# Performance work log

Measured on AMD Instinct MI355X. Metric: run time of the kernel, lower is better.

## Reference

```python
import jax, jax.numpy as jnp
import numpy as np

EPS = 1e-12  # F.normalize eps


def setup_inputs() -> dict:
    key = jax.random.key(0)
    ks = jax.random.split(key, 12)
    N_NODES, N_EDGES, VOCAB, D = 100000, 1600000, 200000, 128
    return {
        "ent_embs": jax.random.normal(ks[0], (VOCAB, D), dtype=jnp.float32),
        "rel_embs": jax.random.normal(ks[1], (500, D), dtype=jnp.float32),
        "e_r_bias": jax.random.normal(ks[2], (N_NODES, D), dtype=jnp.float32),
        "out_norm": jax.random.uniform(ks[3], (N_NODES, 1), dtype=jnp.float32),
        "weight_neighbor": jax.random.normal(ks[4], (D, D), dtype=jnp.float32) * 0.05,
        "gru_w_ih": jax.random.normal(ks[5], (3 * D, 2 * D), dtype=jnp.float32) * 0.05,
        "gru_w_hh": jax.random.normal(ks[6], (3 * D, D), dtype=jnp.float32) * 0.05,
        "gru_b_ih": jnp.zeros((3 * D,), dtype=jnp.float32),
        "gru_b_hh": jnp.zeros((3 * D,), dtype=jnp.float32),
        "node_id": jax.random.randint(ks[7], (N_NODES,), 0, VOCAB, dtype=jnp.int64) if jax.config.jax_enable_x64 else jax.random.randint(ks[7], (N_NODES,), 0, VOCAB).astype(jnp.int32),
        "edge_src": jax.random.randint(ks[8], (N_EDGES,), 0, N_NODES).astype(jnp.int32),
        "edge_dst": jax.random.randint(ks[9], (N_EDGES,), 0, N_NODES).astype(jnp.int32),
        "g_idx": 0,
    }


def gru_cell(x, h, w_ih, w_hh, b_ih, b_hh):
    # torch.nn.GRUCell semantics; gates stacked as [r, z, n]
    gx = x @ w_ih.T + b_ih            # [N, 3D]
    gh = h @ w_hh.T + b_hh            # [N, 3D]
    xr, xz, xn = jnp.split(gx, 3, axis=1)
    hr, hz, hn = jnp.split(gh, 3, axis=1)
    r = jax.nn.sigmoid(xr + hr)
    z = jax.nn.sigmoid(xz + hz)
    n = jnp.tanh(xn + r * hn)
    return (1.0 - z) * n + z * h


def reference(ent_embs, rel_embs, e_r_bias, out_norm, weight_neighbor,
              gru_w_ih, gru_w_hh, gru_b_ih, gru_b_hh,
              node_id, edge_src, edge_dst, g_idx):
    n_nodes = e_r_bias.shape[0]
    # gather node embeddings, transform once per node (equivalent to per-edge mm)
    h = ent_embs[node_id]                       # [N, D]
    hW = h @ weight_neighbor                    # [N, D]
    msg = hW[edge_src]                          # [E, D] per-edge message
    agg = jax.ops.segment_sum(msg, edge_dst, num_segments=n_nodes)  # scatter-sum
    agg = agg * out_norm                        # apply_func: elementwise norm scale
    x = jnp.concatenate([agg, e_r_bias], axis=1)  # [N, 2D]
    # g_idx == 0 branch: hidden state is e_r_bias
    h0 = gru_cell(x, e_r_bias, gru_w_ih, gru_w_hh, gru_b_ih, gru_b_hh)
    h0 = jax.nn.relu(h0)
    # dropout is identity in eval mode
    norm = jnp.maximum(jnp.linalg.norm(h0, axis=1, keepdims=True), EPS)
    return h0 / norm
```

## Files before the change

### kernel.cpp

```cpp
#include <hip/hip_runtime.h>
#include <hip/hip_bf16.h>

#define D 128

typedef unsigned short u16;
typedef unsigned int   u32;
typedef unsigned long long u64;
typedef short bf16x8 __attribute__((ext_vector_type(8)));
typedef float f32x4  __attribute__((ext_vector_type(4)));

__device__ __forceinline__ float bf2f(u16 u) {
    union { u32 i; float f; } v; v.i = ((u32)u) << 16; return v.f;
}
__device__ __forceinline__ float bflo(u32 p) {
    union { u32 i; float f; } v; v.i = p << 16; return v.f;
}
__device__ __forceinline__ float bfhi(u32 p) {
    union { u32 i; float f; } v; v.i = p & 0xffff0000u; return v.f;
}
__device__ __forceinline__ u16 f2bf(float f) {
    union { float f; u32 i; } v; v.f = f;
    return (u16)((v.i + 0x7fffu + ((v.i >> 16) & 1u)) >> 16);
}
__device__ __forceinline__ float ldf(const void* p, long i, int isb) {
    return isb ? bf2f(((const u16*)p)[i]) : ((const float*)p)[i];
}

__device__ __forceinline__ float sigm(float x) { return 1.0f / (1.0f + __expf(-x)); }
__device__ __forceinline__ float tanh_fast(float x) {
    float a = fabsf(x);
    float t = __expf(-2.0f * a);
    float r = (1.0f - t) / (1.0f + t);
    return copysignf(r, x);
}

__global__ void DRlocal_net_79173427135059_kernel() {}

__global__ __launch_bounds__(64) void k_detect(const void* ent, const void* nid,
                                               int* flag, int* bhist) {
    int lane = threadIdx.x;
    for (int i = lane; i < 512; i += 64) bhist[i] = 0;
    float a = fabsf(bf2f(((const u16*)ent)[lane]));
    bool sane = (a >= 9.765625e-4f && a <= 64.0f);
    u64 m = __ballot(sane);
    u32 w = ((const u32*)nid)[lane];
    bool oddzero = ((lane & 1) == 0) || (w == 0u);
    u64 m2 = __ballot(oddzero);
    if (lane == 0) {
        flag[0] = (__popcll(m) >= 48) ? 1 : 0;
        flag[1] = (m2 == ~0ull) ? 1 : 0;
    }
}

__global__ __launch_bounds__(256) void k_prep(
    const void* __restrict__ w_ih, const void* __restrict__ w_hh,
    const void* __restrict__ b_ih, const void* __restrict__ b_hh,
    const void* __restrict__ W, const int* __restrict__ flag,
    u16* __restrict__ WTb, u16* __restrict__ Wihb, u16* __restrict__ Whhb,
    float* __restrict__ bif, float* __restrict__ bhf)
{
    int isb = flag[0];
    int t = blockIdx.x * 256 + threadIdx.x;
    if (t < 16384) {
        int k = t >> 7, j = t & 127;
        u16 v = isb ? ((const u16*)W)[t] : f2bf(((const float*)W)[t]);
        WTb[j * 128 + k] = v;
        return;
    }
    int u = t - 16384;
    if (u < 98304) { Wihb[u] = isb ? ((const u16*)w_ih)[u] : f2bf(((const float*)w_ih)[u]); return; }
    int v = u - 98304;
    if (v < 49152) { Whhb[v] = isb ? ((const u16*)w_hh)[v] : f2bf(((const float*)w_hh)[v]); return; }
    int b = v - 49152;
    if (b < 384) { bif[b] = ldf(b_ih, b, isb); return; }
    int c = b - 384;
    if (c < 384) { bhf[c] = ldf(b_hh, c, isb); return; }
}

__global__ __launch_bounds__(256) void k_gmm_mfma(
    const void* __restrict__ ent, const void* __restrict__ node_id,
    const u16* __restrict__ WTb, u16* __restrict__ hW,
    const int* __restrict__ flag, int N)
{
    int isb = flag[0], i64 = flag[1];
    int tid = threadIdx.x;
    int wave = tid >> 6, lane = tid & 63;
    int qm = lane >> 4, qr = lane & 15;
    int row0 = blockIdx.x * 64 + wave * 16;

    int rowA = row0 + qr; if (rowA >= N) rowA = N - 1;
    long nid = i64 ? (long)((const long long*)node_id)[rowA]
                   : (long)((const int*)node_id)[rowA];

    bf16x8 a[4];
    if (isb) {
        const u16* ep = (const u16*)ent + nid * 128 + qm * 8;
        #pragma unroll
        for (int s = 0; s < 4; ++s) a[s] = *(const bf16x8*)(ep + s * 32);
    } else {
        const float* ep = (const float*)ent + nid * 128 + qm * 8;
        #pragma unroll
        for (int s = 0; s < 4; ++s) {
            float4 f0 = *(const float4*)(ep + s * 32);
            float4 f1 = *(const float4*)(ep + s * 32 + 4);
            bf16x8 t;
            t[0] = (short)f2bf(f0.x); t[1] = (short)f2bf(f0.y);
            t[2] = (short)f2bf(f0.z); t[3] = (short)f2bf(f0.w);
            t[4] = (short)f2bf(f1.x); t[5] = (short)f2bf(f1.y);
            t[6] = (short)f2bf(f1.z); t[7] = (short)f2bf(f1.w);
            a[s] = t;
        }
    }

    int r0 = row0 + qm * 4;
    #pragma unroll
    for (int f = 0; f < 8; ++f) {
        f32x4 acc = {0.f, 0.f, 0.f, 0.f};
        const u16* wp = WTb + (size_t)(f * 16 + qr) * 128 + qm * 8;
        #pragma unroll
        for (int s = 0; s < 4; ++s) {
            bf16x8 b = *(const bf16x8*)(wp + s * 32);
            acc = __builtin_amdgcn_mfma_f32_16x16x32_bf16(a[s], b, acc, 0, 0, 0);
        }
        int col = f * 16 + qr;
        #pragma unroll
        for (int r = 0; r < 4; ++r) {
            int row = r0 + r;
            if (row < N) hW[(size_t)row * 128 + col] = f2bf(acc[r]);
        }
    }
}


__global__ __launch_bounds__(256) void k_bhist(
    const int* __restrict__ edst, int* __restrict__ bhist,
    int E, int NB, int bshift)
{
    __shared__ int lcnt[512];
    int t = threadIdx.x;
    int e0 = blockIdx.x * 8192;
    for (int i = t; i < NB; i += 256) lcnt[i] = 0;
    __syncthreads();
    for (int i = t; i < 8192; i += 256) {
        int e = e0 + i;
        if (e < E) atomicAdd(&lcnt[edst[e] >> bshift], 1);
    }
    __syncthreads();
    for (int i = t; i < NB; i += 256) {
        int c = lcnt[i];
        if (c) atomicAdd(&bhist[i], c);
    }
}

__global__ __launch_bounds__(512) void k_bscan(
    const int* __restrict__ bhist, int* __restrict__ bstart,
    int* __restrict__ bcur, int* __restrict__ rowstart,
    int NB, int N, int E)
{
    __shared__ int sh[512];
    int t = threadIdx.x;
    int v = (t < NB) ? bhist[t] : 0;
    sh[t] = v;
    __syncthreads();
    #pragma unroll
    for (int off = 1; off < 512; off <<= 1) {
        int x = (t >= off) ? sh[t - off] : 0;
        __syncthreads();
        sh[t] += x;
        __syncthreads();
    }
    int excl = sh[t] - v;
    if (t < NB) { bstart[t] = excl; bcur[t] = excl; }
    if (t == 0) { bstart[NB] = E; rowstart[N] = E; }
}

__global__ __launch_bounds__(256) void k_afill(
    const int* __restrict__ esrc, const int* __restrict__ edst,
    int* __restrict__ bcur, u64* __restrict__ ebuf,
    int E, int NB, int bshift)
{
    __shared__ int lcnt[512];
    int t = threadIdx.x;
    int e0 = blockIdx.x * 8192;
    for (int i = t; i < NB; i += 256) lcnt[i] = 0;
    __syncthreads();
    for (int i = t; i < 8192; i += 256) {
        int e = e0 + i;
        if (e < E) atomicAdd(&lcnt[edst[e] >> bshift], 1);
    }
    __syncthreads();
    for (int b = t; b < NB; b += 256) {
        int c = lcnt[b];
        lcnt[b] = c ? atomicAdd(&bcur[b], c) : 0;
    }
    __syncthreads();
    for (int i = t; i < 8192; i += 256) {
        int e = e0 + i;
        if (e < E) {
            int d = edst[e];
            int pos = atomicAdd(&lcnt[d >> bshift], 1);
            ebuf[pos] = ((u64)(u32)esrc[e] << 32) | (u32)d;
        }
    }
}

__global__ __launch_bounds__(256) void k_bfill(
    const u64* __restrict__ ebuf, const int* __restrict__ bstart,
    int* __restrict__ rowstart, int* __restrict__ sorted_src,
    int N, int bshift)
{
    __shared__ int lcnt[1024];
    __shared__ int lscan[256];
    int b = blockIdx.x, t = threadIdx.x;
    int nodes = 1 << bshift;
    int per = nodes >> 8;
    int base = b << bshift;
    int beg = bstart[b], end = bstart[b + 1];

    for (int i = t; i < nodes; i += 256) lcnt[i] = 0;
    __syncthreads();
    for (int i = beg + t; i < end; i += 256) {
        int d = (int)(u32)ebuf[i];
        atomicAdd(&lcnt[d - base], 1);
    }
    __syncthreads();

    int myv[4]; int mysum = 0;
    #pragma unroll
    for (int j = 0; j < 4; ++j) {
        myv[j] = (j < per) ? lcnt[t * per + j] : 0;
        mysum += myv[j];
    }
    lscan[t] = mysum;
    __syncthreads();
    #pragma unroll
    for (int off = 1; off < 256; off <<= 1) {
        int x = (t >= off) ? lscan[t - off] : 0;
        __syncthreads();
        lscan[t] += x;
        __syncthreads();
    }
    int run = beg + lscan[t] - mysum;
    #pragma unroll
    for (int j = 0; j < 4; ++j) {
        if (j < per) {
            int idx = t * per + j;
            int node = base + idx;
            if (node < N) rowstart[node] = run;
            lcnt[idx] = run;
            run += myv[j];
        }
    }
    __syncthreads();
    for (int i = beg + t; i < end; i += 256) {
        u64 p = ebuf[i];
        int d = (int)(u32)p;
        int pos = atomicAdd(&lcnt[d - base], 1);
        sorted_src[pos] = (int)(p >> 32);
    }
}

__global__ __launch_bounds__(256) void k_seg(
    const u16* __restrict__ hW, const int* __restrict__ rowstart,
    const int* __restrict__ sorted_src, const void* __restrict__ onorm,
    const void* __restrict__ bias, u16* __restrict__ X,
    const int* __restrict__ flag, int N)
{
    int isb = flag[0];
    int tid = threadIdx.x;
    int node = blockIdx.x * 4 + (tid >> 6);
    int lane = tid & 63;
    if (node >= N) return;
    int beg = rowstart[node], end = rowstart[node + 1];
    const u32* hw2 = (const u32*)hW;
    float a0 = 0.f, a1 = 0.f;
    int e = beg;
    for (; e + 8 <= end; e += 8) {
        int sI[8]; u32 vI[8];
        #pragma unroll
        for (int i = 0; i < 8; ++i) sI[i] = sorted_src[e + i];
        #pragma unroll
        for (int i = 0; i < 8; ++i) vI[i] = hw2[(size_t)sI[i] * 64 + lane];
        #pragma unroll
        for (int i = 0; i < 8; ++i) { a0 += bflo(vI[i]); a1 += bfhi(vI[i]); }
    }
    for (; e + 4 <= end; e += 4) {
        int s0 = sorted_src[e], s1 = sorted_src[e + 1];
        int s2 = sorted_src[e + 2], s3 = sorted_src[e + 3];
        u32 v0 = hw2[(size_t)s0 * 64 + lane];
        u32 v1 = hw2[(size_t)s1 * 64 + lane];
        u32 v2 = hw2[(size_t)s2 * 64 + lane];
        u32 v3 = hw2[(size_t)s3 * 64 + lane];
        a0 += bflo(v0) + bflo(v1) + bflo(v2) + bflo(v3);
        a1 += bfhi(v0) + bfhi(v1) + bfhi(v2) + bfhi(v3);
    }
    for (; e < end; ++e) {
        u32 v = hw2[(size_t)sorted_src[e] * 64 + lane];
        a0 += bflo(v); a1 += bfhi(v);
    }
    float on = ldf(onorm, node, isb);
    u32 p = ((u32)f2bf(a1 * on) << 16) | (u32)f2bf(a0 * on);
    ((u32*)X)[(size_t)node * 128 + lane] = p;
    u32 pb;
    if (isb) pb = ((const u32*)bias)[(size_t)node * 64 + lane];
    else {
        const float* bp = (const float*)bias + (size_t)node * 128 + lane * 2;
        pb = ((u32)f2bf(bp[1]) << 16) | (u32)f2bf(bp[0]);
    }
    ((u32*)X)[(size_t)node * 128 + 64 + lane] = pb;
}

__global__ __launch_bounds__(512, 2) void k_gru_mfma(
    const u16* __restrict__ X, const u16* __restrict__ Wih,
    const u16* __restrict__ Whh, const float* __restrict__ bif,
    const float* __restrict__ bhf, void* __restrict__ out,
    float* __restrict__ ssb,
    const int* __restrict__ flag, int N, int NpadX)
{
    __shared__ alignas(16) char smem[147456];
    int isb = flag[0];
    int tid = threadIdx.x;
    int wave = tid >> 6, lane = tid & 63;
    int qm = lane >> 4, qr = lane & 15;
    int g = blockIdx.x & 1;
    int chunk = blockIdx.x >> 1;
    int g64 = g * 64;

    for (int t = tid; t < 6144; t += 512) {
        int L = t * 16;
        int kb = L & 511;
        int c  = (L >> 9) & 63;
        int gi = L >> 15;
        int src = (gi * 128 + g64 + c) * 512 + kb;
        int dst = L ^ ((c & 7) << 4);
        *(bf16x8*)(smem + dst) = *(const bf16x8*)((const char*)Wih + src);
    }
    for (int t = tid; t < 3072; t += 512) {
        int L = t * 16;
        int kb = L & 255;
        int c  = (L >> 8) & 63;
        int gi = L >> 14;
        int src = (gi * 128 + g64 + c) * 256 + kb;
        int dst = 98304 + (L ^ ((c & 7) << 4));
        *(bf16x8*)(smem + dst) = *(const bf16x8*)((const char*)Whh + src);
    }
    __syncthreads();

    int rbase = chunk * 256 + wave * 32;

    bf16x8 aA[8], aB[8];
    {
        const u16* x0 = X + (size_t)(rbase + qr) * 256 + qm * 8;
        #pragma unroll
        for (int s = 0; s < 8; ++s) aA[s] = *(const bf16x8*)(x0 + s * 32);
        const u16* x1 = x0 + 16 * 256;
        #pragma unroll
        for (int s = 0; s < 8; ++s) aB[s] = *(const bf16x8*)(x1 + s * 32);
    }

    float ss[8] = {0.f, 0.f, 0.f, 0.f, 0.f, 0.f, 0.f, 0.f};

    #pragma unroll 1
    for (int sl = 0; sl < 4; ++sl) {
        int colIdx = sl * 16 + qr;
        int colg = g64 + colIdx;
        int sw = (qr & 7) << 4;
        int cbI = colIdx * 512 + qm * 16;
        int cbH = colIdx * 256 + qm * 16;

        f32x4 zz = {0.f, 0.f, 0.f, 0.f};
        f32x4 aR0 = zz, aR1 = zz, aZ0 = zz, aZ1 = zz;
        f32x4 aN0 = zz, aN1 = zz, aH0 = zz, aH1 = zz;

        {
            bf16x8 w[12];
            #pragma unroll
            for (int s = 0; s < 8; ++s)
                w[s] = *(const bf16x8*)(smem + ((cbI + s * 64) ^ sw));
            #pragma unroll
            for (int s = 0; s < 4; ++s)
                w[8 + s] = *(const bf16x8*)(smem + 98304 + ((cbH + s * 64) ^ sw));
            #pragma unroll
            for (int s = 0; s < 8; ++s) {
                aR0 = __builtin_amdgcn_mfma_f32_16x16x32_bf16(aA[s], w[s], aR0, 0, 0, 0);
                aR1 = __builtin_amdgcn_mfma_f32_16x16x32_bf16(aB[s], w[s], aR1, 0, 0, 0);
            }
            #pragma unroll
            for (int s = 0; s < 4; ++s) {
                aR0 = __builtin_amdgcn_mfma_f32_16x16x32_bf16(aA[4 + s], w[8 + s], aR0, 0, 0, 0);
                aR1 = __builtin_amdgcn_mfma_f32_16x16x32_bf16(aB[4 + s], w[8 + s], aR1, 0, 0, 0);
            }
        }
        {
            bf16x8 w[12];
            #pragma unroll
            for (int s = 0; s < 8; ++s)
                w[s] = *(const bf16x8*)(smem + 32768 + ((cbI + s * 64) ^ sw));
            #pragma unroll
            for (int s = 0; s < 4; ++s)
                w[8 + s] = *(const bf16x8*)(smem + 98304 + 16384 + ((cbH + s * 64) ^ sw));
            #pragma unroll
            for (int s = 0; s < 8; ++s) {
                aZ0 = __builtin_amdgcn_mfma_f32_16x16x32_bf16(aA[s], w[s], aZ0, 0, 0, 0);
                aZ1 = __builtin_amdgcn_mfma_f32_16x16x32_bf16(aB[s], w[s], aZ1, 0, 0, 0);
            }
            #pragma unroll
            for (int s = 0; s < 4; ++s) {
                aZ0 = __builtin_amdgcn_mfma_f32_16x16x32_bf16(aA[4 + s], w[8 + s], aZ0, 0, 0, 0);
                aZ1 = __builtin_amdgcn_mfma_f32_16x16x32_bf16(aB[4 + s], w[8 + s], aZ1, 0, 0, 0);
            }
        }
        {
            bf16x8 w[12];
            #pragma unroll
            for (int s = 0; s < 8; ++s)
                w[s] = *(const bf16x8*)(smem + 65536 + ((cbI + s * 64) ^ sw));
            #pragma unroll
            for (int s = 0; s < 4; ++s)
                w[8 + s] = *(const bf16x8*)(smem + 98304 + 32768 + ((cbH + s * 64) ^ sw));
            #pragma unroll
            for (int s = 0; s < 8; ++s) {
                aN0 = __builtin_amdgcn_mfma_f32_16x16x32_bf16(aA[s], w[s], aN0, 0, 0, 0);
                aN1 = __builtin_amdgcn_mfma_f32_16x16x32_bf16(aB[s], w[s], aN1, 0, 0, 0);
            }
            #pragma unroll
            for (int s = 0; s < 4; ++s) {
                aH0 = __builtin_amdgcn_mfma_f32_16x16x32_bf16(aA[4 + s], w[8 + s], aH0, 0, 0, 0);
                aH1 = __builtin_amdgcn_mfma_f32_16x16x32_bf16(aB[4 + s], w[8 + s], aH1, 0, 0, 0);
            }
        }

        float brz = bif[colg] + bhf[colg];
        float bzz = bif[128 + colg] + bhf[128 + colg];
        float bnx = bif[256 + colg];
        float bnh = bhf[256 + colg];

        #pragma unroll
        for (int ms = 0; ms < 2; ++ms) {
            #pragma unroll
            for (int r = 0; r < 4; ++r) {
                float vR = ms ? aR1[r] : aR0[r];
                float vZ = ms ? aZ1[r] : aZ0[r];
                float vN = ms ? aN1[r] : aN0[r];
                float vH = ms ? aH1[r] : aH0[r];
                int row = rbase + ms * 16 + qm * 4 + r;
                float rg = sigm(vR + brz);
                float z  = sigm(vZ + bzz);
                float ng = tanh_fast(vN + bnx + rg * (vH + bnh));
                float h  = bf2f(X[(size_t)row * 256 + 128 + colg]);
                float h0 = fmaxf((1.f - z) * ng + z * h, 0.f);
                if (row < N) {
                    if (isb) ((u16*)out)[(size_t)row * 128 + colg] = f2bf(h0);
                    else     ((float*)out)[(size_t)row * 128 + colg] = h0;
                }
                ss[ms * 4 + r] += h0 * h0;
            }
        }
    }

    #pragma unroll
    for (int i = 0; i < 8; ++i) {
        float s = ss[i];
        s += __shfl_xor(s, 1, 64);
        s += __shfl_xor(s, 2, 64);
        s += __shfl_xor(s, 4, 64);
        s += __shfl_xor(s, 8, 64);
        ss[i] = s;
    }
    if (qr == 0) {
        #pragma unroll
        for (int ms = 0; ms < 2; ++ms)
            #pragma unroll
            for (int r = 0; r < 4; ++r)
                ssb[(size_t)g * NpadX + rbase + ms * 16 + qm * 4 + r] = ss[ms * 4 + r];
    }
}

__global__ __launch_bounds__(256) void k_norm(
    void* __restrict__ out, const float* __restrict__ ssb,
    const int* __restrict__ flag, int N, int NpadX)
{
    int isb = flag[0];
    int tid = threadIdx.x;
    int wave = tid >> 6, lane = tid & 63;
    int row = blockIdx.x * 16 + wave * 4 + (lane >> 4);
    if (row >= N) return;
    int c8 = (lane & 15) * 8;
    float s = ssb[row] + ssb[(size_t)NpadX + row];
    float iv = 1.f / fmaxf(sqrtf(s), 1e-12f);
    if (isb) {
        u16* p = (u16*)out + (size_t)row * 128 + c8;
        bf16x8 v = *(const bf16x8*)p;
        bf16x8 o;
        #pragma unroll
        for (int j = 0; j < 8; ++j) o[j] = (short)f2bf(bf2f((u16)v[j]) * iv);
        *(bf16x8*)p = o;
    } else {
        float* p = (float*)out + (size_t)row * 128 + c8;
        float4 v0 = *(float4*)p, v1 = *(float4*)(p + 4);
        v0.x *= iv; v0.y *= iv; v0.z *= iv; v0.w *= iv;
        v1.x *= iv; v1.y *= iv; v1.z *= iv; v1.w *= iv;
        *(float4*)p = v0; *(float4*)(p + 4) = v1;
    }
}

extern "C" void kernel_launch(void* const* d_in, const int* in_sizes, int n_in,
                              void* d_out, int out_size, void* d_ws, size_t ws_size,
                              hipStream_t stream) {
    const void* ent     = d_in[0];
    const void* bias    = d_in[2];
    const void* onorm   = d_in[3];
    const void* W       = d_in[4];
    const void* w_ih    = d_in[5];
    const void* w_hh    = d_in[6];
    const void* b_ih    = d_in[7];
    const void* b_hh    = d_in[8];
    const void* node_id = d_in[9];
    const int*  esrc    = (const int*)d_in[10];
    const int*  edst    = (const int*)d_in[11];

    int N = in_sizes[2] / D;
    int E = in_sizes[10];
    int NpadX = ((N + 255) / 256) * 256;

    int bshift = 8;
    while ((((N - 1) >> bshift) + 1) > 512) bshift++;
    int NB = ((N - 1) >> bshift) + 1;

    char* ws = (char*)d_ws;
    size_t o = 0;
    int*   flag = (int*)(ws + o);   o += 64;
    u16*   WTb  = (u16*)(ws + o);   o += 16384u * 2;
    u16*   Wihb = (u16*)(ws + o);   o += 98304u * 2;
    u16*   Whhb = (u16*)(ws + o);   o += 49152u * 2;
    float* bif  = (float*)(ws + o); o += 2048;
    float* bhf  = (float*)(ws + o); o += 2048;
    u16*   X    = (u16*)(ws + o);   o += (size_t)NpadX * 256 * 2;
    u16*   hW   = (u16*)(ws + o);   o += (size_t)N * D * 2;
    int*   bhist = (int*)(ws + o);  o += 512 * 4;
    int*   bstart = (int*)(ws + o); o += 514 * 4;
    int*   bcur  = (int*)(ws + o);  o += 512 * 4;
    int*   rowstart = (int*)(ws + o); o += ((size_t)N + 16) * 4;
    int*   sorted_src = (int*)(ws + o); o += (size_t)E * 4;
    u64*   ebuf = (u64*)X;
    float* ssb = (float*)sorted_src;

    int nchunk = NpadX / 256;
    int nA = (E + 8191) / 8192;

    k_detect<<<1, 64, 0, stream>>>(ent, node_id, flag, bhist);
    k_prep<<<643, 256, 0, stream>>>(w_ih, w_hh, b_ih, b_hh, W, flag,
                                    WTb, Wihb, Whhb, bif, bhf);
    k_gmm_mfma<<<(N + 63) / 64, 256, 0, stream>>>(ent, node_id, WTb, hW, flag, N);
    k_bhist<<<nA, 256, 0, stream>>>(edst, bhist, E, NB, bshift);
    k_bscan<<<1, 512, 0, stream>>>(bhist, bstart, bcur, rowstart, NB, N, E);
    k_afill<<<nA, 256, 0, stream>>>(esrc, edst, bcur, ebuf, E, NB, bshift);
    k_bfill<<<NB, 256, 0, stream>>>(ebuf, bstart, rowstart, sorted_src, N, bshift);
    k_seg<<<(N + 3) / 4, 256, 0, stream>>>(hW, rowstart, sorted_src, onorm, bias, X, flag, N);
    k_gru_mfma<<<nchunk * 2, 512, 0, stream>>>(X, Wihb, Whhb, bif, bhf, d_out, ssb, flag, N, NpadX);
    k_norm<<<(N + 15) / 16, 256, 0, stream>>>(d_out, ssb, flag, N, NpadX);
}
```

Before: 508.1 us.

## Split segment-sum gather into column slices with 8 edges per wave

Restructures the CSR segment-sum kernel. Each block now handles one 8-column slice (8 u32 = 16 bf16) for a group of 32 nodes, and each wave processes 8 edges in parallel with 8 lanes per edge, then reduces across lanes with shuffles. Previously each wave read a full 256-byte row per edge, one edge at a time. The new layout gives more independent gathers in flight per wave and may concentrate each block's cache footprint on one column slice. In exchange, each gather is only 32 contiguous bytes, sorted_src is re-read 8 times (once per column slice), and shuffle reductions are added.

```diff
diff --git a/kernel.cpp b/kernel.cpp
--- a/kernel.cpp
+++ b/kernel.cpp
@@ -131,7 +131,6 @@
     }
 }
 
-
 __global__ __launch_bounds__(256) void k_bhist(
     const int* __restrict__ edst, int* __restrict__ bhist,
     int E, int NB, int bshift)
@@ -268,46 +267,42 @@
 {
     int isb = flag[0];
     int tid = threadIdx.x;
-    int node = blockIdx.x * 4 + (tid >> 6);
-    int lane = tid & 63;
-    if (node >= N) return;
-    int beg = rowstart[node], end = rowstart[node + 1];
+    int wave = tid >> 6, lane = tid & 63;
+    int le = lane >> 3;
+    int lc = lane & 7;
+    int sl = blockIdx.x & 7;
+    int ngrp = blockIdx.x >> 3;
+    int u0 = sl * 8 + lc;
+
     const u32* hw2 = (const u32*)hW;
-    float a0 = 0.f, a1 = 0.f;
-    int e = beg;
-    for (; e + 8 <= end; e += 8) {
-        int sI[8]; u32 vI[8];
-        #pragma unroll
-        for (int i = 0; i < 8; ++i) sI[i] = sorted_src[e + i];
-        #pragma unroll
-        for (int i = 0; i < 8; ++i) vI[i] = hw2[(size_t)sI[i] * 64 + lane];
-        #pragma unroll
-        for (int i = 0; i < 8; ++i) { a0 += bflo(vI[i]); a1 += bfhi(vI[i]); }
-    }
-    for (; e + 4 <= end; e += 4) {
-        int s0 = sorted_src[e], s1 = sorted_src[e + 1];
-        int s2 = sorted_src[e + 2], s3 = sorted_src[e + 3];
-        u32 v0 = hw2[(size_t)s0 * 64 + lane];
-        u32 v1 = hw2[(size_t)s1 * 64 + lane];
-        u32 v2 = hw2[(size_t)s2 * 64 + lane];
-        u32 v3 = hw2[(size_t)s3 * 64 + lane];
-        a0 += bflo(v0) + bflo(v1) + bflo(v2) + bflo(v3);
-        a1 += bfhi(v0) + bfhi(v1) + bfhi(v2) + bfhi(v3);
-    }
-    for (; e < end; ++e) {
-        u32 v = hw2[(size_t)sorted_src[e] * 64 + lane];
-        a0 += bflo(v); a1 += bfhi(v);
-    }
-    float on = ldf(onorm, node, isb);
-    u32 p = ((u32)f2bf(a1 * on) << 16) | (u32)f2bf(a0 * on);
-    ((u32*)X)[(size_t)node * 128 + lane] = p;
-    u32 pb;
-    if (isb) pb = ((const u32*)bias)[(size_t)node * 64 + lane];
-    else {
-        const float* bp = (const float*)bias + (size_t)node * 128 + lane * 2;
-        pb = ((u32)f2bf(bp[1]) << 16) | (u32)f2bf(bp[0]);
-    }
-    ((u32*)X)[(size_t)node * 128 + 64 + lane] = pb;
+
+    #pragma unroll 1
+    for (int ni = wave; ni < 32; ni += 4) {
+        int node = ngrp * 32 + ni;
+        if (node >= N) break;
+        int beg = rowstart[node], end = rowstart[node + 1];
+        float a0 = 0.f, a1 = 0.f;
+        for (int e = beg + le; e < end; e += 8) {
+            int src = sorted_src[e];
+            u32 v = hw2[(size_t)src * 64 + u0];
+            a0 += bflo(v); a1 += bfhi(v);
+        }
+        a0 += __shfl_xor(a0, 8, 64);  a1 += __shfl_xor(a1, 8, 64);
+        a0 += __shfl_xor(a0, 16, 64); a1 += __shfl_xor(a1, 16, 64);
+        a0 += __shfl_xor(a0, 32, 64); a1 += __shfl_xor(a1, 32, 64);
+        if (le == 0) {
+            float on = ldf(onorm, node, isb);
+            u32 p = ((u32)f2bf(a1 * on) << 16) | (u32)f2bf(a0 * on);
+            ((u32*)X)[(size_t)node * 128 + u0] = p;
+            u32 pb;
+            if (isb) pb = ((const u32*)bias)[(size_t)node * 64 + u0];
+            else {
+                const float* bp = (const float*)bias + (size_t)node * 128 + u0 * 2;
+                pb = ((u32)f2bf(bp[1]) << 16) | (u32)f2bf(bp[0]);
+            }
+            ((u32*)X)[(size_t)node * 128 + 64 + u0] = pb;
+        }
+    }
 }
 
 __global__ __launch_bounds__(512, 2) void k_gru_mfma(
@@ -556,7 +551,7 @@
     k_bscan<<<1, 512, 0, stream>>>(bhist, bstart, bcur, rowstart, NB, N, E);
     k_afill<<<nA, 256, 0, stream>>>(esrc, edst, bcur, ebuf, E, NB, bshift);
     k_bfill<<<NB, 256, 0, stream>>>(ebuf, bstart, rowstart, sorted_src, N, bshift);
-    k_seg<<<(N + 3) / 4, 256, 0, stream>>>(hW, rowstart, sorted_src, onorm, bias, X, flag, N);
+    k_seg<<<((N + 31) / 32) * 8, 256, 0, stream>>>(hW, rowstart, sorted_src, onorm, bias, X, flag, N);
     k_gru_mfma<<<nchunk * 2, 512, 0, stream>>>(X, Wihb, Whhb, bif, bhf, d_out, ssb, flag, N, NpadX);
     k_norm<<<(N + 15) / 16, 256, 0, stream>>>(d_out, ssb, flag, N, NpadX);
 }
```

New measurement: 793.7 us. 1.56x slower.
